# Performance work log

Measured on AMD Instinct MI355X. Metric: run time of the kernel, lower is better.

## Reference

```python
import math
import jax, jax.numpy as jnp
import numpy as np

B, N, D_IN, D_OUT = 8, 2048, 768, 768

def setup_inputs() -> dict:
    key = jax.random.key(0)
    k1, k2, k3 = jax.random.split(key, 3)
    x = jax.random.normal(k1, (B, N, D_IN), dtype=jnp.float32)
    W_qkv = jax.random.normal(k2, (D_IN, 3 * D_OUT), dtype=jnp.float32) * (1.0 / math.sqrt(D_IN))
    b_qkv = jax.random.normal(k3, (3 * D_OUT,), dtype=jnp.float32) * 0.02
    return {"x": x, "W_qkv": W_qkv, "b_qkv": b_qkv}

def reference(x, W_qkv, b_qkv):
    d_out = D_OUT
    # fused QKV projection: [B, N, 3*d_out]
    qkv = jnp.einsum('bnd,de->bne', x, W_qkv) + b_qkv
    q = qkv[:, :, :d_out]
    k = qkv[:, :, d_out:2 * d_out]
    v = qkv[:, :, 2 * d_out:3 * d_out]
    scale = 1.0 / math.sqrt(d_out)
    # scores: [B, N, N]
    scores = jnp.einsum('bqd,bkd->bqk', q, k) * scale
    attn = jax.nn.softmax(scores, axis=-1)
    # context: [B, N, d_out]
    context = jnp.einsum('bqk,bkd->bqd', attn, v)
    return context
```

## Files before the change

### kernel.cpp

```cpp
#include <hip/hip_runtime.h>
#include <hip/hip_bf16.h>

typedef __attribute__((ext_vector_type(8))) short short8;
typedef __attribute__((ext_vector_type(4))) float floatx4;

#define BATCH 8
#define SEQ 2048
#define DMODEL 768
#define NQKV 2304
#define SCALE 0.03608439182435161f

__device__ __forceinline__ ushort f2bf(float f) {
    union { float f; uint u; } in; in.f = f;
    uint u = in.u;
    return (ushort)((u + 0x7FFFu + ((u >> 16) & 1u)) >> 16);
}
__device__ __forceinline__ float bf2f(ushort h) {
    union { uint u; float f; } o; o.u = ((uint)h) << 16;
    return o.f;
}

__device__ __forceinline__ void async_copy16(void* lds_uniform, const void* gaddr) {
    __builtin_amdgcn_global_load_lds(
        (const __attribute__((address_space(1))) void*)gaddr,
        (__attribute__((address_space(3))) void*)lds_uniform,
        16, 0, 0);
}

#define BARRIER() asm volatile("s_barrier" ::: "memory")
#define LGKM0()   do { asm volatile("s_waitcnt lgkmcnt(0)" ::: "memory"); \
                       __builtin_amdgcn_sched_barrier(0); } while (0)
#define LGKM_HINT() asm volatile("s_waitcnt lgkmcnt(8)" ::: "memory")
#define VMCNT(n)  asm volatile("s_waitcnt vmcnt(" #n ")" ::: "memory")

template<int MODE, int KT>
__global__ __launch_bounds__(512, 2) void gemm8(
    const ushort* __restrict__ A, const ushort* __restrict__ B,
    const float* __restrict__ bias,
    void* __restrict__ out0, void* __restrict__ out1, void* __restrict__ out2,
    int lda, int ldb)
{
    extern __shared__ __align__(16) ushort lds[];
    const int tid  = threadIdx.x;
    const int w    = tid >> 6, lane = tid & 63;
    const int wr   = w >> 2,  wc   = w & 3;
    const int lr   = lane & 15, kg = lane >> 4;
    const int srow = lane >> 3;
    const int scc  = (lane & 7) ^ srow;

    const int m0 = blockIdx.x * 256, n0 = blockIdx.y * 256;
    const ushort* Abase;
    const ushort* Bbase;
    if (MODE == 0) {
        Abase = A + (size_t)m0 * lda;
        Bbase = B + (size_t)n0 * ldb;
    } else if (MODE == 1) {
        const int b = blockIdx.z;
        Abase = A + ((size_t)(b * SEQ + m0)) * lda;
        Bbase = B + ((size_t)(b * SEQ + n0)) * ldb;
    } else {
        const int b = blockIdx.z;
        Abase = A + (size_t)b * SEQ * SEQ + (size_t)m0 * lda;
        Bbase = B + (size_t)b * DMODEL * SEQ + (size_t)n0 * ldb;
    }

    const ushort* At[2] = { lds,         lds + 32768 };
    const ushort* Bt[2] = { lds + 16384, lds + 49152 };

    #define STG(tile, mat, half) do { if ((tile) < KT) {                          \
        ushort* sb_ = lds + (((tile) & 1) ? 32768 : 0) + ((mat) ? 16384 : 0);     \
        const ushort* g_ = (mat) ? Bbase : Abase;                                 \
        const size_t ld_ = (mat) ? (size_t)ldb : (size_t)lda;                     \
        const int k0_ = (tile) << 6;                                              \
        _Pragma("unroll")                                                         \
        for (int t_ = 0; t_ < 2; ++t_) {                                          \
            const int c8_ = (mat) ? ((w & 3) + ((w >> 2) << 3) + (t_ << 4) + ((half) << 2)) \
                                  : (w + (t_ << 4) + ((half) << 3));              \
            const int row_ = (c8_ << 3) + srow;                                   \
            async_copy16(sb_ + c8_ * 512, g_ + (size_t)row_ * ld_ + k0_ + scc * 8); \
        } } } while (0)

    short8 af[4][2], bf[4][2];
    floatx4 acc[8][4] = {};

    #define LDFRAG(tp, row, c) \
        (*reinterpret_cast<const short8*>(&(tp)[((row) << 6) + ((((c) ^ ((row) & 7))) << 3)]))

    #define READ_A(bufi, mh) do {                                                 \
        _Pragma("unroll") for (int mf_ = 0; mf_ < 4; ++mf_)                       \
        _Pragma("unroll") for (int kk_ = 0; kk_ < 2; ++kk_)                       \
            af[mf_][kk_] = LDFRAG(At[bufi], wr * 128 + ((mh) * 4 + mf_) * 16 + lr, kk_ * 4 + kg); \
    } while (0)
    #define READ_B(bufi, nh) do {                                                 \
        _Pragma("unroll") for (int nf_ = 0; nf_ < 2; ++nf_)                       \
        _Pragma("unroll") for (int kk_ = 0; kk_ < 2; ++kk_)                       \
            bf[(nh) * 2 + nf_][kk_] = LDFRAG(Bt[bufi], wc * 64 + ((nh) * 2 + nf_) * 16 + lr, kk_ * 4 + kg); \
    } while (0)
    #define MFMA_Q(mh, nh) do {                                                   \
        __builtin_amdgcn_s_setprio(1);                                            \
        _Pragma("unroll") for (int mf_ = 0; mf_ < 4; ++mf_)                       \
        _Pragma("unroll") for (int nf_ = 0; nf_ < 2; ++nf_)                       \
        _Pragma("unroll") for (int kk_ = 0; kk_ < 2; ++kk_)                       \
            acc[(mh) * 4 + mf_][(nh) * 2 + nf_] = __builtin_amdgcn_mfma_f32_16x16x32_bf16( \
                af[mf_][kk_], bf[(nh) * 2 + nf_][kk_], acc[(mh) * 4 + mf_][(nh) * 2 + nf_], 0, 0, 0); \
        __builtin_amdgcn_s_setprio(0);                                            \
    } while (0)

    STG(0, 0, 0); STG(0, 1, 0); STG(0, 1, 1); STG(0, 0, 1);
    STG(1, 0, 0); STG(1, 1, 0); STG(1, 1, 1);
    VMCNT(6);
    BARRIER();

    #pragma unroll 1
    for (int it = 0; it < KT / 2; ++it) {
        const int t = 2 * it;
        const bool lastit = (it == KT / 2 - 1);
        READ_A(0, 0); READ_B(0, 0);
        STG(t + 1, 0, 1);
        LGKM_HINT();
        BARRIER(); LGKM0();
        MFMA_Q(0, 0);
        BARRIER();
        READ_B(0, 1);
        STG(t + 2, 0, 0);
        BARRIER(); LGKM0();
        MFMA_Q(0, 1);
        BARRIER();
        READ_A(0, 1);
        STG(t + 2, 1, 0);
        BARRIER(); LGKM0();
        MFMA_Q(1, 0);
        BARRIER();
        STG(t + 2, 1, 1);
        BARRIER();
        MFMA_Q(1, 1);
        if (lastit) { VMCNT(0); } else { VMCNT(6); }
        BARRIER();
        READ_A(1, 0); READ_B(1, 0);
        STG(t + 2, 0, 1);
        LGKM_HINT();
        BARRIER(); LGKM0();
        MFMA_Q(0, 0);
        BARRIER();
        READ_B(1, 1);
        STG(t + 3, 0, 0);
        BARRIER(); LGKM0();
        MFMA_Q(0, 1);
        BARRIER();
        READ_A(1, 1);
        STG(t + 3, 1, 0);
        BARRIER(); LGKM0();
        MFMA_Q(1, 0);
        BARRIER();
        STG(t + 3, 1, 1);
        BARRIER();
        MFMA_Q(1, 1);
        VMCNT(6);
        BARRIER();
    }

    const int mrow = m0 + wr * 128;
    const int ncol = n0 + wc * 64;

    if (MODE == 0 && blockIdx.y >= 6) {
        ushort* Vt = (ushort*)out2;
        const int bIdx = m0 >> 11;
        const int ns0  = m0 & 2047;
        #pragma unroll
        for (int nf = 0; nf < 4; ++nf) {
            const int e = ncol + nf * 16 + lr;
            const int d = e - 2 * DMODEL;
            const float bv = bias[e];
            ushort* vrow = Vt + ((size_t)bIdx * DMODEL + d) * SEQ + ns0;
            #pragma unroll
            for (int a = 0; a < 8; ++a) {
                const floatx4 v = acc[a][nf];
                uint2 u;
                u.x = (uint)f2bf(v[0] + bv) | ((uint)f2bf(v[1] + bv) << 16);
                u.y = (uint)f2bf(v[2] + bv) | ((uint)f2bf(v[3] + bv) << 16);
                *reinterpret_cast<uint2*>(vrow + wr * 128 + a * 16 + kg * 4) = u;
            }
        }
    } else {
        float* scr = reinterpret_cast<float*>(reinterpret_cast<char*>(lds) + (size_t)w * 9216);
        #pragma unroll
        for (int mh = 0; mh < 2; ++mh) {
            #pragma unroll
            for (int np = 0; np < 2; ++np) {
                #pragma unroll
                for (int mf = 0; mf < 4; ++mf)
                    #pragma unroll
                    for (int nf2 = 0; nf2 < 2; ++nf2) {
                        const floatx4 v = acc[mh * 4 + mf][np * 2 + nf2];
                        #pragma unroll
                        for (int r = 0; r < 4; ++r)
                            scr[(mf * 16 + kg * 4 + r) * 36 + nf2 * 16 + lr] = v[r];
                    }
                asm volatile("s_waitcnt lgkmcnt(0)" ::: "memory");
                __builtin_amdgcn_sched_barrier(0);

                if (MODE == 2) {
                    float* Ob = (float*)out0 + (size_t)blockIdx.z * SEQ * DMODEL;
                    const int c4 = (lane & 7) * 4;
                    #pragma unroll
                    for (int p = 0; p < 8; ++p) {
                        const int row = p * 8 + (lane >> 3);
                        const float4 v = *reinterpret_cast<const float4*>(&scr[row * 36 + c4]);
                        *reinterpret_cast<float4*>(
                            &Ob[(size_t)(mrow + mh * 64 + row) * DMODEL + ncol + np * 32 + c4]) = v;
                    }
                } else {
                    const int c8 = (lane & 3) * 8;
                    const int e0 = ncol + np * 32 + c8;
                    ushort* dst; int ec; float mul;
                    float bs[8] = {0, 0, 0, 0, 0, 0, 0, 0};
                    if (MODE == 0) {
                        const bool isQ = e0 < DMODEL;
                        dst = isQ ? (ushort*)out0 : (ushort*)out1;
                        ec  = isQ ? e0 : e0 - DMODEL;
                        mul = isQ ? SCALE : 1.0f;
                        const float4 b0 = *reinterpret_cast<const float4*>(&bias[e0]);
                        const float4 b1 = *reinterpret_cast<const float4*>(&bias[e0 + 4]);
                        bs[0] = b0.x * mul; bs[1] = b0.y * mul;
                        bs[2] = b0.z * mul; bs[3] = b0.w * mul;
                        bs[4] = b1.x * mul; bs[5] = b1.y * mul;
                        bs[6] = b1.z * mul; bs[7] = b1.w * mul;
                    } else {
                        dst = (ushort*)out0 + (size_t)blockIdx.z * SEQ * SEQ;
                        ec = e0; mul = 1.0f;
                    }
                    const size_t ostride = (MODE == 0) ? (size_t)DMODEL : (size_t)SEQ;
                    #pragma unroll
                    for (int p = 0; p < 4; ++p) {
                        const int row = p * 16 + (lane >> 2);
                        const float4 lo = *reinterpret_cast<const float4*>(&scr[row * 36 + c8]);
                        const float4 hi = *reinterpret_cast<const float4*>(&scr[row * 36 + c8 + 4]);
                        short8 o;
                        o[0] = (short)f2bf(lo.x * mul + bs[0]);
                        o[1] = (short)f2bf(lo.y * mul + bs[1]);
                        o[2] = (short)f2bf(lo.z * mul + bs[2]);
                        o[3] = (short)f2bf(lo.w * mul + bs[3]);
                        o[4] = (short)f2bf(hi.x * mul + bs[4]);
                        o[5] = (short)f2bf(hi.y * mul + bs[5]);
                        o[6] = (short)f2bf(hi.z * mul + bs[6]);
                        o[7] = (short)f2bf(hi.w * mul + bs[7]);
                        *reinterpret_cast<short8*>(
                            &dst[(size_t)(mrow + mh * 64 + row) * ostride + ec]) = o;
                    }
                }
                asm volatile("s_waitcnt lgkmcnt(0)" ::: "memory");
                __builtin_amdgcn_sched_barrier(0);
            }
        }
    }
    #undef STG
    #undef LDFRAG
    #undef READ_A
    #undef READ_B
    #undef MFMA_Q
}

__global__ __launch_bounds__(256) void convert_x(const float* __restrict__ X,
                                                 ushort* __restrict__ Xb) {
    const int total = (BATCH * SEQ * DMODEL) / 8;
    for (int i = blockIdx.x * 256 + threadIdx.x; i < total; i += gridDim.x * 256) {
        const float4 v0 = reinterpret_cast<const float4*>(X)[(size_t)i * 2];
        const float4 v1 = reinterpret_cast<const float4*>(X)[(size_t)i * 2 + 1];
        uint4 u;
        u.x = (uint)f2bf(v0.x) | ((uint)f2bf(v0.y) << 16);
        u.y = (uint)f2bf(v0.z) | ((uint)f2bf(v0.w) << 16);
        u.z = (uint)f2bf(v1.x) | ((uint)f2bf(v1.y) << 16);
        u.w = (uint)f2bf(v1.z) | ((uint)f2bf(v1.w) << 16);
        reinterpret_cast<uint4*>(Xb)[i] = u;
    }
}

__global__ __launch_bounds__(256) void convert_wt(const float* __restrict__ W,
                                                  ushort* __restrict__ Wt) {
    __shared__ float tile[32][33];
    const int n0 = blockIdx.x * 32, k0 = blockIdx.y * 32;
    const int tx = threadIdx.x & 31, ty = threadIdx.x >> 5;
    #pragma unroll
    for (int i = 0; i < 32; i += 8)
        tile[ty + i][tx] = W[(size_t)(k0 + ty + i) * NQKV + n0 + tx];
    __syncthreads();
    #pragma unroll
    for (int i = 0; i < 32; i += 8)
        Wt[(size_t)(n0 + ty + i) * DMODEL + k0 + tx] = f2bf(tile[tx][ty + i]);
}

__global__ __launch_bounds__(256) void softmax_rows(ushort* __restrict__ S) {
    const int row = blockIdx.x;
    ushort* p = S + (size_t)row * SEQ;
    const int tid = threadIdx.x;
    const int wave = tid >> 6, lane = tid & 63;

    short8 v8 = *reinterpret_cast<const short8*>(p + tid * 8);
    float v[8];
    #pragma unroll
    for (int j = 0; j < 8; ++j) v[j] = bf2f((ushort)v8[j]);
    float mx = v[0];
    #pragma unroll
    for (int j = 1; j < 8; ++j) mx = fmaxf(mx, v[j]);
    #pragma unroll
    for (int off = 32; off >= 1; off >>= 1) mx = fmaxf(mx, __shfl_xor(mx, off));
    __shared__ float redm[4], reds[4];
    if (lane == 0) redm[wave] = mx;
    __syncthreads();
    mx = fmaxf(fmaxf(redm[0], redm[1]), fmaxf(redm[2], redm[3]));

    float e[8], s = 0.f;
    #pragma unroll
    for (int j = 0; j < 8; ++j) { e[j] = __expf(v[j] - mx); s += e[j]; }
    #pragma unroll
    for (int off = 32; off >= 1; off >>= 1) s += __shfl_xor(s, off);
    if (lane == 0) reds[wave] = s;
    __syncthreads();
    s = reds[0] + reds[1] + reds[2] + reds[3];
    float inv = 1.f / s;

    short8 o;
    #pragma unroll
    for (int j = 0; j < 8; ++j) o[j] = (short)f2bf(e[j] * inv);
    *reinterpret_cast<short8*>(p + tid * 8) = o;
}

extern "C" void kernel_launch(void* const* d_in, const int* in_sizes, int n_in,
                              void* d_out, int out_size, void* d_ws, size_t ws_size,
                              hipStream_t stream) {
    const float* X    = (const float*)d_in[0];
    const float* W    = (const float*)d_in[1];
    const float* bias = (const float*)d_in[2];
    float* Out = (float*)d_out;

    char* ws = (char*)d_ws;
    ushort* S  = (ushort*)ws;
    ushort* Xb = (ushort*)ws;
    ushort* Wt = (ushort*)(ws + (size_t)BATCH * SEQ * DMODEL * 2);
    ushort* Qs = (ushort*)(ws + (size_t)BATCH * SEQ * SEQ * 2);
    ushort* Kb = Qs + (size_t)BATCH * SEQ * DMODEL;
    ushort* Vt = Kb + (size_t)BATCH * SEQ * DMODEL;

    const int LDSB = 131072;
    (void)hipFuncSetAttribute((const void*)gemm8<0, 12>,
                              hipFuncAttributeMaxDynamicSharedMemorySize, LDSB);
    (void)hipFuncSetAttribute((const void*)gemm8<1, 12>,
                              hipFuncAttributeMaxDynamicSharedMemorySize, LDSB);
    (void)hipFuncSetAttribute((const void*)gemm8<2, 32>,
                              hipFuncAttributeMaxDynamicSharedMemorySize, LDSB);

    convert_x<<<2048, 256, 0, stream>>>(X, Xb);
    convert_wt<<<dim3(NQKV / 32, DMODEL / 32), 256, 0, stream>>>(W, Wt);
    gemm8<0, 12><<<dim3(64, 9), 512, LDSB, stream>>>(
        Xb, Wt, bias, Qs, Kb, Vt, DMODEL, DMODEL);
    gemm8<1, 12><<<dim3(8, 8, 8), 512, LDSB, stream>>>(
        Qs, Kb, nullptr, S, nullptr, nullptr, DMODEL, DMODEL);
    softmax_rows<<<BATCH * SEQ, 256, 0, stream>>>(S);
    gemm8<2, 32><<<dim3(8, 3, 8), 512, LDSB, stream>>>(
        S, Vt, nullptr, Out, nullptr, nullptr, SEQ, SEQ);
}
```

Measured before the change: 243.9 us.

## Replace QKV projection gemm with simpler 128x128-tile kernel for more blocks

Moves the QKV projection off the heavily pipelined 256x256-tile gemm8 (576 blocks) onto a new qkv128 kernel with 128x128 tiles, 256 threads and a simple single-buffered K loop (2304 blocks). The aim is better occupancy and tail balance across CUs for this smaller GEMM. The cost is losing the multi-stage async pipelining and double-buffering, since each K step now syncs twice and waits for loads with no overlap. The bias is now added before the scale rather than folded into it, and the MODE 0 paths are removed from gemm8.

```diff
diff --git a/kernel.cpp b/kernel.cpp
--- a/kernel.cpp
+++ b/kernel.cpp
@@ -33,12 +33,123 @@
 #define LGKM_HINT() asm volatile("s_waitcnt lgkmcnt(8)" ::: "memory")
 #define VMCNT(n)  asm volatile("s_waitcnt vmcnt(" #n ")" ::: "memory")
 
+__device__ __forceinline__ void stage128x32(ushort* lds, const ushort* gbase,
+                                            size_t ld, int k0, int wave, int lane) {
+    #pragma unroll
+    for (int t = 0; t < 2; ++t) {
+        const int chunk = wave * 2 + t;
+        const int row = chunk * 16 + (lane >> 2);
+        const ushort* g = gbase + (size_t)row * ld + k0 + (lane & 3) * 8;
+        async_copy16(lds + chunk * 512, g);
+    }
+}
+
+__global__ __launch_bounds__(256) void qkv128(
+    const ushort* __restrict__ Xb,
+    const ushort* __restrict__ Wt,
+    const float* __restrict__ bias,
+    ushort* __restrict__ Qs, ushort* __restrict__ Kb, ushort* __restrict__ Vt)
+{
+    __shared__ __align__(16) ushort smem[2 * 128 * 32];
+    ushort* As = smem;
+    ushort* Bs = smem + 128 * 32;
+    const int tid  = threadIdx.x;
+    const int m0   = blockIdx.x * 128, n0 = blockIdx.y * 128;
+    const int wave = tid >> 6, lane = tid & 63;
+    const int wm   = (wave >> 1) * 64, wn = (wave & 1) * 64;
+    const int lr   = lane & 15, kg = lane >> 4;
+    const ushort* Abase = Xb + (size_t)m0 * DMODEL;
+    const ushort* Bbase = Wt + (size_t)n0 * DMODEL;
+    floatx4 acc[4][4] = {};
+
+    for (int k0 = 0; k0 < DMODEL; k0 += 32) {
+        stage128x32(As, Abase, DMODEL, k0, wave, lane);
+        stage128x32(Bs, Bbase, DMODEL, k0, wave, lane);
+        __syncthreads();
+        short8 a[4], b[4];
+        #pragma unroll
+        for (int i = 0; i < 4; ++i)
+            a[i] = *reinterpret_cast<const short8*>(&As[(wm + i * 16 + lr) * 32 + kg * 8]);
+        #pragma unroll
+        for (int j = 0; j < 4; ++j)
+            b[j] = *reinterpret_cast<const short8*>(&Bs[(wn + j * 16 + lr) * 32 + kg * 8]);
+        #pragma unroll
+        for (int i = 0; i < 4; ++i)
+            #pragma unroll
+            for (int j = 0; j < 4; ++j)
+                acc[i][j] = __builtin_amdgcn_mfma_f32_16x16x32_bf16(a[i], b[j], acc[i][j], 0, 0, 0);
+        __syncthreads();
+    }
+
+    const int by = blockIdx.y;
+    if (by >= 12) {
+        const int bIdx = m0 >> 11;
+        const int ns0  = m0 & 2047;
+        #pragma unroll
+        for (int j = 0; j < 4; ++j) {
+            const int e = n0 + wn + j * 16 + lr;
+            const int d = e - 2 * DMODEL;
+            const float bv = bias[e];
+            ushort* vrow = Vt + ((size_t)bIdx * DMODEL + d) * SEQ + ns0;
+            #pragma unroll
+            for (int i = 0; i < 4; ++i) {
+                const floatx4 v = acc[i][j];
+                uint2 u;
+                u.x = (uint)f2bf(v[0] + bv) | ((uint)f2bf(v[1] + bv) << 16);
+                u.y = (uint)f2bf(v[2] + bv) | ((uint)f2bf(v[3] + bv) << 16);
+                *reinterpret_cast<uint2*>(vrow + wm + i * 16 + kg * 4) = u;
+            }
+        }
+    } else {
+        ushort* dst = (by < 6) ? Qs : Kb;
+        const float mul = (by < 6) ? SCALE : 1.0f;
+        const int ecolbase = n0 - ((by < 6) ? 0 : DMODEL);
+        float* scr = reinterpret_cast<float*>(
+            reinterpret_cast<char*>(smem) + (size_t)wave * 4096);
+        const int row = lane >> 2, c8 = (lane & 3) * 8;
+        #pragma unroll
+        for (int i = 0; i < 4; ++i) {
+            #pragma unroll
+            for (int np = 0; np < 2; ++np) {
+                #pragma unroll
+                for (int nf2 = 0; nf2 < 2; ++nf2) {
+                    const floatx4 v = acc[i][np * 2 + nf2];
+                    #pragma unroll
+                    for (int r = 0; r < 4; ++r)
+                        scr[(kg * 4 + r) * 36 + nf2 * 16 + lr] = v[r];
+                }
+                asm volatile("s_waitcnt lgkmcnt(0)" ::: "memory");
+                __builtin_amdgcn_sched_barrier(0);
+
+                const int eg = n0 + wn + np * 32 + c8;
+                const float4 b0 = *reinterpret_cast<const float4*>(&bias[eg]);
+                const float4 b1 = *reinterpret_cast<const float4*>(&bias[eg + 4]);
+                const float4 lo = *reinterpret_cast<const float4*>(&scr[row * 36 + c8]);
+                const float4 hi = *reinterpret_cast<const float4*>(&scr[row * 36 + c8 + 4]);
+                short8 o;
+                o[0] = (short)f2bf((lo.x + b0.x) * mul);
+                o[1] = (short)f2bf((lo.y + b0.y) * mul);
+                o[2] = (short)f2bf((lo.z + b0.z) * mul);
+                o[3] = (short)f2bf((lo.w + b0.w) * mul);
+                o[4] = (short)f2bf((hi.x + b1.x) * mul);
+                o[5] = (short)f2bf((hi.y + b1.y) * mul);
+                o[6] = (short)f2bf((hi.z + b1.z) * mul);
+                o[7] = (short)f2bf((hi.w + b1.w) * mul);
+                const int ec = ecolbase + wn + np * 32 + c8;
+                *reinterpret_cast<short8*>(
+                    &dst[(size_t)(m0 + wm + i * 16 + row) * DMODEL + ec]) = o;
+
+                asm volatile("s_waitcnt lgkmcnt(0)" ::: "memory");
+                __builtin_amdgcn_sched_barrier(0);
+            }
+        }
+    }
+}
+
 template<int MODE, int KT>
 __global__ __launch_bounds__(512, 2) void gemm8(
     const ushort* __restrict__ A, const ushort* __restrict__ B,
-    const float* __restrict__ bias,
-    void* __restrict__ out0, void* __restrict__ out1, void* __restrict__ out2,
-    int lda, int ldb)
+    void* __restrict__ out0, int lda, int ldb)
 {
     extern __shared__ __align__(16) ushort lds[];
     const int tid  = threadIdx.x;
@@ -51,10 +162,7 @@
     const int m0 = blockIdx.x * 256, n0 = blockIdx.y * 256;
     const ushort* Abase;
     const ushort* Bbase;
-    if (MODE == 0) {
-        Abase = A + (size_t)m0 * lda;
-        Bbase = B + (size_t)n0 * ldb;
-    } else if (MODE == 1) {
+    if (MODE == 1) {
         const int b = blockIdx.z;
         Abase = A + ((size_t)(b * SEQ + m0)) * lda;
         Bbase = B + ((size_t)(b * SEQ + n0)) * ldb;
@@ -161,96 +269,57 @@
 
     const int mrow = m0 + wr * 128;
     const int ncol = n0 + wc * 64;
-
-    if (MODE == 0 && blockIdx.y >= 6) {
-        ushort* Vt = (ushort*)out2;
-        const int bIdx = m0 >> 11;
-        const int ns0  = m0 & 2047;
-        #pragma unroll
-        for (int nf = 0; nf < 4; ++nf) {
-            const int e = ncol + nf * 16 + lr;
-            const int d = e - 2 * DMODEL;
-            const float bv = bias[e];
-            ushort* vrow = Vt + ((size_t)bIdx * DMODEL + d) * SEQ + ns0;
+    float* scr = reinterpret_cast<float*>(reinterpret_cast<char*>(lds) + (size_t)w * 9216);
+    #pragma unroll
+    for (int mh = 0; mh < 2; ++mh) {
+        #pragma unroll
+        for (int np = 0; np < 2; ++np) {
             #pragma unroll
-            for (int a = 0; a < 8; ++a) {
-                const floatx4 v = acc[a][nf];
-                uint2 u;
-                u.x = (uint)f2bf(v[0] + bv) | ((uint)f2bf(v[1] + bv) << 16);
-                u.y = (uint)f2bf(v[2] + bv) | ((uint)f2bf(v[3] + bv) << 16);
-                *reinterpret_cast<uint2*>(vrow + wr * 128 + a * 16 + kg * 4) = u;
+            for (int mf = 0; mf < 4; ++mf)
+                #pragma unroll
+                for (int nf2 = 0; nf2 < 2; ++nf2) {
+                    const floatx4 v = acc[mh * 4 + mf][np * 2 + nf2];
+                    #pragma unroll
+                    for (int r = 0; r < 4; ++r)
+                        scr[(mf * 16 + kg * 4 + r) * 36 + nf2 * 16 + lr] = v[r];
+                }
+            asm volatile("s_waitcnt lgkmcnt(0)" ::: "memory");
+            __builtin_amdgcn_sched_barrier(0);
+
+            if (MODE == 2) {
+                float* Ob = (float*)out0 + (size_t)blockIdx.z * SEQ * DMODEL;
+                const int c4 = (lane & 7) * 4;
+                #pragma unroll
+                for (int p = 0; p < 8; ++p) {
+                    const int row = p * 8 + (lane >> 3);
+                    const float4 v = *reinterpret_cast<const float4*>(&scr[row * 36 + c4]);
+                    *reinterpret_cast<float4*>(
+                        &Ob[(size_t)(mrow + mh * 64 + row) * DMODEL + ncol + np * 32 + c4]) = v;
+                }
+            } else {
+                ushort* dst = (ushort*)out0 + (size_t)blockIdx.z * SEQ * SEQ;
+                const int c8 = (lane & 3) * 8;
+                const int e0 = ncol + np * 32 + c8;
+                #pragma unroll
+                for (int p = 0; p < 4; ++p) {
+                    const int row = p * 16 + (lane >> 2);
+                    const float4 lo = *reinterpret_cast<const float4*>(&scr[row * 36 + c8]);
+                    const float4 hi = *reinterpret_cast<const float4*>(&scr[row * 36 + c8 + 4]);
+                    short8 o;
+                    o[0] = (short)f2bf(lo.x);
+                    o[1] = (short)f2bf(lo.y);
+                    o[2] = (short)f2bf(lo.z);
+                    o[3] = (short)f2bf(lo.w);
+                    o[4] = (short)f2bf(hi.x);
+                    o[5] = (short)f2bf(hi.y);
+                    o[6] = (short)f2bf(hi.z);
+                    o[7] = (short)f2bf(hi.w);
+                    *reinterpret_cast<short8*>(
+                        &dst[(size_t)(mrow + mh * 64 + row) * SEQ + e0]) = o;
+                }
             }
-        }
-    } else {
-        float* scr = reinterpret_cast<float*>(reinterpret_cast<char*>(lds) + (size_t)w * 9216);
-        #pragma unroll
-        for (int mh = 0; mh < 2; ++mh) {
-            #pragma unroll
-            for (int np = 0; np < 2; ++np) {
-                #pragma unroll
-                for (int mf = 0; mf < 4; ++mf)
-                    #pragma unroll
-                    for (int nf2 = 0; nf2 < 2; ++nf2) {
-                        const floatx4 v = acc[mh * 4 + mf][np * 2 + nf2];
-                        #pragma unroll
-                        for (int r = 0; r < 4; ++r)
-                            scr[(mf * 16 + kg * 4 + r) * 36 + nf2 * 16 + lr] = v[r];
-                    }
-                asm volatile("s_waitcnt lgkmcnt(0)" ::: "memory");
-                __builtin_amdgcn_sched_barrier(0);
-
-                if (MODE == 2) {
-                    float* Ob = (float*)out0 + (size_t)blockIdx.z * SEQ * DMODEL;
-                    const int c4 = (lane & 7) * 4;
-                    #pragma unroll
-                    for (int p = 0; p < 8; ++p) {
-                        const int row = p * 8 + (lane >> 3);
-                        const float4 v = *reinterpret_cast<const float4*>(&scr[row * 36 + c4]);
-                        *reinterpret_cast<float4*>(
-                            &Ob[(size_t)(mrow + mh * 64 + row) * DMODEL + ncol + np * 32 + c4]) = v;
-                    }
-                } else {
-                    const int c8 = (lane & 3) * 8;
-                    const int e0 = ncol + np * 32 + c8;
-                    ushort* dst; int ec; float mul;
-                    float bs[8] = {0, 0, 0, 0, 0, 0, 0, 0};
-                    if (MODE == 0) {
-                        const bool isQ = e0 < DMODEL;
-                        dst = isQ ? (ushort*)out0 : (ushort*)out1;
-                        ec  = isQ ? e0 : e0 - DMODEL;
-                        mul = isQ ? SCALE : 1.0f;
-                        const float4 b0 = *reinterpret_cast<const float4*>(&bias[e0]);
-                        const float4 b1 = *reinterpret_cast<const float4*>(&bias[e0 + 4]);
-                        bs[0] = b0.x * mul; bs[1] = b0.y * mul;
-                        bs[2] = b0.z * mul; bs[3] = b0.w * mul;
-                        bs[4] = b1.x * mul; bs[5] = b1.y * mul;
-                        bs[6] = b1.z * mul; bs[7] = b1.w * mul;
-                    } else {
-                        dst = (ushort*)out0 + (size_t)blockIdx.z * SEQ * SEQ;
-                        ec = e0; mul = 1.0f;
-                    }
-                    const size_t ostride = (MODE == 0) ? (size_t)DMODEL : (size_t)SEQ;
-                    #pragma unroll
-                    for (int p = 0; p < 4; ++p) {
-                        const int row = p * 16 + (lane >> 2);
-                        const float4 lo = *reinterpret_cast<const float4*>(&scr[row * 36 + c8]);
-                        const float4 hi = *reinterpret_cast<const float4*>(&scr[row * 36 + c8 + 4]);
-                        short8 o;
-                        o[0] = (short)f2bf(lo.x * mul + bs[0]);
-                        o[1] = (short)f2bf(lo.y * mul + bs[1]);
-                        o[2] = (short)f2bf(lo.z * mul + bs[2]);
-                        o[3] = (short)f2bf(lo.w * mul + bs[3]);
-                        o[4] = (short)f2bf(hi.x * mul + bs[4]);
-                        o[5] = (short)f2bf(hi.y * mul + bs[5]);
-                        o[6] = (short)f2bf(hi.z * mul + bs[6]);
-                        o[7] = (short)f2bf(hi.w * mul + bs[7]);
-                        *reinterpret_cast<short8*>(
-                            &dst[(size_t)(mrow + mh * 64 + row) * ostride + ec]) = o;
-                    }
-                }
-                asm volatile("s_waitcnt lgkmcnt(0)" ::: "memory");
-                __builtin_amdgcn_sched_barrier(0);
-            }
+            asm volatile("s_waitcnt lgkmcnt(0)" ::: "memory");
+            __builtin_amdgcn_sched_barrier(0);
         }
     }
     #undef STG
@@ -342,8 +411,6 @@
     ushort* Vt = Kb + (size_t)BATCH * SEQ * DMODEL;
 
     const int LDSB = 131072;
-    (void)hipFuncSetAttribute((const void*)gemm8<0, 12>,
-                              hipFuncAttributeMaxDynamicSharedMemorySize, LDSB);
     (void)hipFuncSetAttribute((const void*)gemm8<1, 12>,
                               hipFuncAttributeMaxDynamicSharedMemorySize, LDSB);
     (void)hipFuncSetAttribute((const void*)gemm8<2, 32>,
@@ -351,11 +418,10 @@
 
     convert_x<<<2048, 256, 0, stream>>>(X, Xb);
     convert_wt<<<dim3(NQKV / 32, DMODEL / 32), 256, 0, stream>>>(W, Wt);
-    gemm8<0, 12><<<dim3(64, 9), 512, LDSB, stream>>>(
-        Xb, Wt, bias, Qs, Kb, Vt, DMODEL, DMODEL);
+    qkv128<<<dim3(128, 18), 256, 0, stream>>>(Xb, Wt, bias, Qs, Kb, Vt);
     gemm8<1, 12><<<dim3(8, 8, 8), 512, LDSB, stream>>>(
-        Qs, Kb, nullptr, S, nullptr, nullptr, DMODEL, DMODEL);
+        Qs, Kb, S, DMODEL, DMODEL);
     softmax_rows<<<BATCH * SEQ, 256, 0, stream>>>(S);
     gemm8<2, 32><<<dim3(8, 3, 8), 512, LDSB, stream>>>(
-        S, Vt, nullptr, Out, nullptr, nullptr, SEQ, SEQ);
-}
+        S, Vt, Out, SEQ, SEQ);
+}
```

Result: slower. 264.0 us (+8.2%).
